# Optimization experiments

Hardware: AMD Instinct MI355X
Metric: run time of the kernel (lower is better)

The kernel has to match this reference:

```python
import jax, jax.numpy as jnp
import numpy as np

B, S, H = 128, 512, 1024
SEP = 2


def setup_inputs() -> dict:
    key = jax.random.key(0)
    k1, k2, k3, k4 = jax.random.split(key, 4)
    hidden_states = jax.random.normal(k1, (B, S, H), dtype=jnp.float32)
    # per-sample segment boundaries: <s> title </s></s> lead </s> pad...
    title_end = jax.random.randint(k2, (B,), 5, 200)          # pos of first </s>
    lead_end = jax.random.randint(k3, (B,), 250, S - 2)        # pos of third </s>
    tokens = jax.random.randint(k4, (B, S), 5, 64000)          # avoid SEP=2 collisions
    rows = jnp.arange(B)
    input_ids = tokens.at[:, 0].set(0)                          # <s>
    input_ids = input_ids.at[rows, title_end].set(SEP)
    input_ids = input_ids.at[rows, title_end + 1].set(SEP)
    input_ids = input_ids.at[rows, lead_end].set(SEP)
    attention_mask = (jnp.arange(S)[None, :] <= lead_end[:, None]).astype(jnp.int32)
    return {
        "hidden_states": hidden_states,
        "input_ids": input_ids.astype(jnp.int64),
        "attention_mask": attention_mask,
        "sep_token_id": SEP,
    }


def reference(hidden_states, input_ids, attention_mask, sep_token_id):
    # hidden_states: (B,S,H); input_ids, attention_mask: (B,S)
    b, s, h = hidden_states.shape
    sep = input_ids == sep_token_id                      # (B,S) bool
    cnt = jnp.cumsum(sep.astype(jnp.int32), axis=1)      # inclusive sep count
    num_seps = cnt[:, -1]                                # (B,)

    def pos_of(k):
        # index of k-th separator (argmax of first True); 0 if absent
        return jnp.argmax(sep & (cnt == k), axis=1)

    p1, p2, p3 = pos_of(1), pos_of(2), pos_of(3)
    mask_len = attention_mask.sum(axis=1)
    lead_end = jnp.where(num_seps >= 3, p3, mask_len)    # (B,)
    lead_start = p2 + 1

    idx = jnp.arange(s)[None, :]                         # (1,S)
    valid = (num_seps >= 2)[:, None]
    title_mask = (idx >= 1) & (idx < p1[:, None]) & valid
    lead_mask = (idx >= lead_start[:, None]) & (idx < lead_end[:, None]) & valid

    cls = hidden_states[:, 0, :]                         # fallback: <s> token

    def masked_mean(m):
        mf = m.astype(hidden_states.dtype)               # (B,S)
        ssum = jnp.einsum('bs,bsh->bh', mf, hidden_states)
        c = mf.sum(axis=1, keepdims=True)                # (B,1)
        return jnp.where(c > 0, ssum / jnp.maximum(c, 1.0), cls)

    return masked_mean(title_mask), masked_mean(lead_mask)
```

## Files before the change

kernel.cpp:

```cpp
#include <hip/hip_runtime.h>

#define BB 128
#define SS 512
#define HH 1024
#define CHUNKS 16
#define SCHUNK (SS / CHUNKS)

__device__ __forceinline__ int4 compute_meta(const int* __restrict__ ids,
                                             const int* __restrict__ attn,
                                             int b, int sep) {
    __shared__ unsigned long long words[SS / 64];
    __shared__ int sh_p[4];
    __shared__ int sh_mask;
    const int t = threadIdx.x;
    const int* row = ids + b * SS;
    const int tok0 = row[t];
    const int tok1 = row[t + 256];
    const unsigned long long b0 = __ballot(tok0 == sep);
    const unsigned long long b1 = __ballot(tok1 == sep);
    if ((t & 63) == 0) {
        words[t >> 6] = b0;
        words[4 + (t >> 6)] = b1;
    }
    if (t == 0) sh_mask = 0;
    __syncthreads();
    if (t == 0) {
        int cnt = 0, p1 = 0, p2 = 0, p3 = 0;
        for (int i = 0; i < SS / 64; ++i) {
            unsigned long long word = words[i];
            while (word && cnt < 3) {
                const int pos = i * 64 + __builtin_ctzll(word);
                ++cnt;
                if (cnt == 1) p1 = pos;
                else if (cnt == 2) p2 = pos;
                else p3 = pos;
                word &= word - 1;
            }
        }
        sh_p[0] = p1; sh_p[1] = p2; sh_p[2] = p3; sh_p[3] = cnt;
    }
    __syncthreads();
    const int cnt = sh_p[3];
    if (cnt < 3) {
        const int* arow = attn + b * SS;
        atomicAdd(&sh_mask, arow[t] + arow[t + 256]);
        __syncthreads();
    }
    int4 m;
    if (cnt >= 2) {
        m.x = 1;
        m.y = max(sh_p[0], 1);
        m.z = sh_p[1] + 1;
        const int e = (cnt >= 3) ? sh_p[2] : sh_mask;
        m.w = max(e, m.z);
    } else {
        m.x = 0; m.y = 0; m.z = 0; m.w = 0;
    }
    return m;
}

__device__ __forceinline__ void acc4(float4& a, const float4 v) {
    a.x += v.x; a.y += v.y; a.z += v.z; a.w += v.w;
}

__global__ void seg_sum_partial(const float* __restrict__ hs,
                                const int* __restrict__ ids,
                                const int* __restrict__ attn,
                                const int* __restrict__ sep_tok,
                                float* __restrict__ partials) {
    const int c = blockIdx.x;
    const int b = blockIdx.y;
    const int4 m = compute_meta(ids, attn, b, sep_tok[0]);

    const int cbeg = c * SCHUNK, cend = cbeg + SCHUNK;
    const int t0 = max(m.x, cbeg), t1 = min(m.y, cend);
    const int l0 = max(m.z, cbeg), l1 = min(m.w, cend);
    const bool ht = t1 > t0, hl = l1 > l0;
    if (!ht && !hl) return;

    const int h4 = threadIdx.x;
    const float4* base = (const float4*)(hs + (size_t)b * SS * HH);
    float4* pbase = (float4*)(partials + (size_t)(b * CHUNKS + c) * 2 * HH);

    if (ht) {
        float4 a = {0.f, 0.f, 0.f, 0.f};
        #pragma unroll 4
        for (int s = t0; s < t1; ++s) acc4(a, base[(size_t)s * (HH / 4) + h4]);
        pbase[h4] = a;
    }
    if (hl) {
        float4 a = {0.f, 0.f, 0.f, 0.f};
        #pragma unroll 4
        for (int s = l0; s < l1; ++s) acc4(a, base[(size_t)s * (HH / 4) + h4]);
        pbase[HH / 4 + h4] = a;
    }
}

__global__ void seg_final_partial(const float* __restrict__ hs,
                                  const int* __restrict__ ids,
                                  const int* __restrict__ attn,
                                  const int* __restrict__ sep_tok,
                                  const float* __restrict__ partials,
                                  float* __restrict__ out) {
    const int span = blockIdx.x;
    const int b = blockIdx.y;
    const int4 m = compute_meta(ids, attn, b, sep_tok[0]);
    const int h4 = threadIdx.x;

    const int s0 = span == 0 ? m.x : m.z;
    const int s1 = span == 0 ? m.y : m.w;

    float4 a = {0.f, 0.f, 0.f, 0.f};
    #pragma unroll
    for (int c = 0; c < CHUNKS; ++c) {
        const int cbeg = c * SCHUNK, cend = cbeg + SCHUNK;
        const int x0 = max(s0, cbeg), x1 = min(s1, cend);
        if (x1 > x0) {
            const float4* p = (const float4*)(partials +
                (size_t)(b * CHUNKS + c) * 2 * HH + (size_t)span * HH);
            acc4(a, p[h4]);
        }
    }

    const int cntr = max(s1 - s0, 0);
    float4 o;
    if (cntr > 0) {
        const float c = (float)cntr;
        o.x = a.x / c; o.y = a.y / c; o.z = a.z / c; o.w = a.w / c;
    } else {
        o = ((const float4*)(hs + (size_t)b * SS * HH))[h4];
    }
    ((float4*)out)[(size_t)(span * BB + b) * (HH / 4) + h4] = o;
}

__global__ void seg_sum_atomic(const float* __restrict__ hs,
                               const int* __restrict__ ids,
                               const int* __restrict__ attn,
                               const int* __restrict__ sep_tok,
                               float* __restrict__ sums) {
    const int c = blockIdx.x;
    const int b = blockIdx.y;
    const int4 m = compute_meta(ids, attn, b, sep_tok[0]);

    const int cbeg = c * SCHUNK, cend = cbeg + SCHUNK;
    const int t0 = max(m.x, cbeg), t1 = min(m.y, cend);
    const int l0 = max(m.z, cbeg), l1 = min(m.w, cend);
    if (t0 >= t1 && l0 >= l1) return;

    const int h4 = threadIdx.x;
    const float4* base = (const float4*)(hs + (size_t)b * SS * HH);
    float* sbase = sums + (size_t)b * 2 * HH;

    if (t1 > t0) {
        float4 a = {0.f, 0.f, 0.f, 0.f};
        #pragma unroll 4
        for (int s = t0; s < t1; ++s) acc4(a, base[(size_t)s * (HH / 4) + h4]);
        atomicAdd(sbase + h4 * 4 + 0, a.x); atomicAdd(sbase + h4 * 4 + 1, a.y);
        atomicAdd(sbase + h4 * 4 + 2, a.z); atomicAdd(sbase + h4 * 4 + 3, a.w);
    }
    if (l1 > l0) {
        float4 a = {0.f, 0.f, 0.f, 0.f};
        #pragma unroll 4
        for (int s = l0; s < l1; ++s) acc4(a, base[(size_t)s * (HH / 4) + h4]);
        float* sl = sbase + HH;
        atomicAdd(sl + h4 * 4 + 0, a.x); atomicAdd(sl + h4 * 4 + 1, a.y);
        atomicAdd(sl + h4 * 4 + 2, a.z); atomicAdd(sl + h4 * 4 + 3, a.w);
    }
}

__global__ void seg_final_atomic(const float* __restrict__ hs,
                                 const int* __restrict__ ids,
                                 const int* __restrict__ attn,
                                 const int* __restrict__ sep_tok,
                                 const float* __restrict__ sums,
                                 float* __restrict__ out) {
    const int span = blockIdx.x;
    const int b = blockIdx.y;
    const int4 m = compute_meta(ids, attn, b, sep_tok[0]);
    const int h4 = threadIdx.x;

    const int s0 = span == 0 ? m.x : m.z;
    const int s1 = span == 0 ? m.y : m.w;
    const int cntr = max(s1 - s0, 0);

    float4 o;
    if (cntr > 0) {
        const float4 a = ((const float4*)(sums + (size_t)b * 2 * HH + (size_t)span * HH))[h4];
        const float c = (float)cntr;
        o.x = a.x / c; o.y = a.y / c; o.z = a.z / c; o.w = a.w / c;
    } else {
        o = ((const float4*)(hs + (size_t)b * SS * HH))[h4];
    }
    ((float4*)out)[(size_t)(span * BB + b) * (HH / 4) + h4] = o;
}

extern "C" void kernel_launch(void* const* d_in, const int* in_sizes, int n_in,
                              void* d_out, int out_size, void* d_ws, size_t ws_size,
                              hipStream_t stream) {
    const float* hs  = (const float*)d_in[0];
    const int*   ids = (const int*)d_in[1];
    const int*   am  = (const int*)d_in[2];
    const int*   sep = (const int*)d_in[3];
    float* out = (float*)d_out;

    const size_t partial_bytes = (size_t)BB * CHUNKS * 2 * HH * sizeof(float);

    if (ws_size >= partial_bytes) {
        float* partials = (float*)d_ws;
        seg_sum_partial<<<dim3(CHUNKS, BB), 256, 0, stream>>>(hs, ids, am, sep, partials);
        seg_final_partial<<<dim3(2, BB), 256, 0, stream>>>(hs, ids, am, sep, partials, out);
    } else {
        float* sums = (float*)d_ws;
        hipMemsetAsync(sums, 0, (size_t)BB * 2 * HH * sizeof(float), stream);
        seg_sum_atomic<<<dim3(CHUNKS, BB), 256, 0, stream>>>(hs, ids, am, sep, sums);
        seg_final_atomic<<<dim3(2, BB), 256, 0, stream>>>(hs, ids, am, sep, sums, out);
    }
}
```

Before: 47.18 us.

## Load-balance segment rows across blocks with strided interleaving and nontemporal loads

```diff
diff --git a/kernel.cpp b/kernel.cpp
--- a/kernel.cpp
+++ b/kernel.cpp
@@ -3,8 +3,9 @@
 #define BB 128
 #define SS 512
 #define HH 1024
-#define CHUNKS 16
-#define SCHUNK (SS / CHUNKS)
+#define NB 16
+
+typedef float f32x4 __attribute__((ext_vector_type(4)));
 
 __device__ __forceinline__ int4 compute_meta(const int* __restrict__ ids,
                                              const int* __restrict__ attn,
@@ -59,139 +60,91 @@
     return m;
 }
 
-__device__ __forceinline__ void acc4(float4& a, const float4 v) {
-    a.x += v.x; a.y += v.y; a.z += v.z; a.w += v.w;
+__device__ __forceinline__ int lead_first_u(int t_len, int nb) {
+    int d = nb - (t_len % NB);
+    if (d < 0) d += NB;
+    return t_len + d;
 }
 
-__global__ void seg_sum_partial(const float* __restrict__ hs,
-                                const int* __restrict__ ids,
-                                const int* __restrict__ attn,
-                                const int* __restrict__ sep_tok,
-                                float* __restrict__ partials) {
-    const int c = blockIdx.x;
-    const int b = blockIdx.y;
+__global__ void seg_sum_balanced(const float* __restrict__ hs,
+                                 const int* __restrict__ ids,
+                                 const int* __restrict__ attn,
+                                 const int* __restrict__ sep_tok,
+                                 float* __restrict__ partials) {
+    const int nb = blockIdx.x;
+    const int b  = blockIdx.y;
     const int4 m = compute_meta(ids, attn, b, sep_tok[0]);
-
-    const int cbeg = c * SCHUNK, cend = cbeg + SCHUNK;
-    const int t0 = max(m.x, cbeg), t1 = min(m.y, cend);
-    const int l0 = max(m.z, cbeg), l1 = min(m.w, cend);
-    const bool ht = t1 > t0, hl = l1 > l0;
-    if (!ht && !hl) return;
+    const int t_len = m.y - m.x;
+    const int l_len = m.w - m.z;
+    const int T = t_len + l_len;
 
     const int h4 = threadIdx.x;
-    const float4* base = (const float4*)(hs + (size_t)b * SS * HH);
-    float4* pbase = (float4*)(partials + (size_t)(b * CHUNKS + c) * 2 * HH);
+    const f32x4* base = (const f32x4*)(hs + (size_t)b * SS * HH);
+    f32x4* p = (f32x4*)(partials + (size_t)(b * NB + nb) * 2 * HH);
 
-    if (ht) {
-        float4 a = {0.f, 0.f, 0.f, 0.f};
-        #pragma unroll 4
-        for (int s = t0; s < t1; ++s) acc4(a, base[(size_t)s * (HH / 4) + h4]);
-        pbase[h4] = a;
+    if (nb < t_len) {
+        f32x4 a = {0.f, 0.f, 0.f, 0.f};
+        #pragma unroll 2
+        for (int u = nb; u < t_len; u += NB) {
+            const int s = m.x + u;
+            a += __builtin_nontemporal_load(&base[(size_t)s * (HH / 4) + h4]);
+        }
+        p[h4] = a;
     }
-    if (hl) {
-        float4 a = {0.f, 0.f, 0.f, 0.f};
-        #pragma unroll 4
-        for (int s = l0; s < l1; ++s) acc4(a, base[(size_t)s * (HH / 4) + h4]);
-        pbase[HH / 4 + h4] = a;
+    const int u0 = lead_first_u(t_len, nb);
+    if (u0 < T) {
+        f32x4 a = {0.f, 0.f, 0.f, 0.f};
+        #pragma unroll 2
+        for (int u = u0; u < T; u += NB) {
+            const int s = m.z + (u - t_len);
+            a += __builtin_nontemporal_load(&base[(size_t)s * (HH / 4) + h4]);
+        }
+        p[HH / 4 + h4] = a;
     }
 }
 
-__global__ void seg_final_partial(const float* __restrict__ hs,
-                                  const int* __restrict__ ids,
-                                  const int* __restrict__ attn,
-                                  const int* __restrict__ sep_tok,
-                                  const float* __restrict__ partials,
-                                  float* __restrict__ out) {
+__global__ void seg_final_balanced(const float* __restrict__ hs,
+                                   const int* __restrict__ ids,
+                                   const int* __restrict__ attn,
+                                   const int* __restrict__ sep_tok,
+                                   const float* __restrict__ partials,
+                                   float* __restrict__ out) {
     const int span = blockIdx.x;
     const int b = blockIdx.y;
     const int4 m = compute_meta(ids, attn, b, sep_tok[0]);
     const int h4 = threadIdx.x;
+    const int t_len = m.y - m.x;
+    const int l_len = m.w - m.z;
+    const int T = t_len + l_len;
 
-    const int s0 = span == 0 ? m.x : m.z;
-    const int s1 = span == 0 ? m.y : m.w;
-
-    float4 a = {0.f, 0.f, 0.f, 0.f};
-    #pragma unroll
-    for (int c = 0; c < CHUNKS; ++c) {
-        const int cbeg = c * SCHUNK, cend = cbeg + SCHUNK;
-        const int x0 = max(s0, cbeg), x1 = min(s1, cend);
-        if (x1 > x0) {
-            const float4* p = (const float4*)(partials +
-                (size_t)(b * CHUNKS + c) * 2 * HH + (size_t)span * HH);
-            acc4(a, p[h4]);
+    f32x4 a = {0.f, 0.f, 0.f, 0.f};
+    int cntr;
+    if (span == 0) {
+        cntr = t_len;
+        const int lim = min(t_len, NB);
+        for (int nb = 0; nb < lim; ++nb) {
+            const f32x4* p = (const f32x4*)(partials + (size_t)(b * NB + nb) * 2 * HH);
+            a += p[h4];
+        }
+    } else {
+        cntr = l_len;
+        #pragma unroll
+        for (int nb = 0; nb < NB; ++nb) {
+            if (lead_first_u(t_len, nb) < T) {
+                const f32x4* p = (const f32x4*)(partials + (size_t)(b * NB + nb) * 2 * HH);
+                a += p[HH / 4 + h4];
+            }
         }
     }
 
-    const int cntr = max(s1 - s0, 0);
-    float4 o;
+    f32x4 o;
     if (cntr > 0) {
         const float c = (float)cntr;
-        o.x = a.x / c; o.y = a.y / c; o.z = a.z / c; o.w = a.w / c;
+        o = a / c;
     } else {
-        o = ((const float4*)(hs + (size_t)b * SS * HH))[h4];
+        o = ((const f32x4*)(hs + (size_t)b * SS * HH))[h4];
     }
-    ((float4*)out)[(size_t)(span * BB + b) * (HH / 4) + h4] = o;
-}
-
-__global__ void seg_sum_atomic(const float* __restrict__ hs,
-                               const int* __restrict__ ids,
-                               const int* __restrict__ attn,
-                               const int* __restrict__ sep_tok,
-                               float* __restrict__ sums) {
-    const int c = blockIdx.x;
-    const int b = blockIdx.y;
-    const int4 m = compute_meta(ids, attn, b, sep_tok[0]);
-
-    const int cbeg = c * SCHUNK, cend = cbeg + SCHUNK;
-    const int t0 = max(m.x, cbeg), t1 = min(m.y, cend);
-    const int l0 = max(m.z, cbeg), l1 = min(m.w, cend);
-    if (t0 >= t1 && l0 >= l1) return;
-
-    const int h4 = threadIdx.x;
-    const float4* base = (const float4*)(hs + (size_t)b * SS * HH);
-    float* sbase = sums + (size_t)b * 2 * HH;
-
-    if (t1 > t0) {
-        float4 a = {0.f, 0.f, 0.f, 0.f};
-        #pragma unroll 4
-        for (int s = t0; s < t1; ++s) acc4(a, base[(size_t)s * (HH / 4) + h4]);
-        atomicAdd(sbase + h4 * 4 + 0, a.x); atomicAdd(sbase + h4 * 4 + 1, a.y);
-        atomicAdd(sbase + h4 * 4 + 2, a.z); atomicAdd(sbase + h4 * 4 + 3, a.w);
-    }
-    if (l1 > l0) {
-        float4 a = {0.f, 0.f, 0.f, 0.f};
-        #pragma unroll 4
-        for (int s = l0; s < l1; ++s) acc4(a, base[(size_t)s * (HH / 4) + h4]);
-        float* sl = sbase + HH;
-        atomicAdd(sl + h4 * 4 + 0, a.x); atomicAdd(sl + h4 * 4 + 1, a.y);
-        atomicAdd(sl + h4 * 4 + 2, a.z); atomicAdd(sl + h4 * 4 + 3, a.w);
-    }
-}
-
-__global__ void seg_final_atomic(const float* __restrict__ hs,
-                                 const int* __restrict__ ids,
-                                 const int* __restrict__ attn,
-                                 const int* __restrict__ sep_tok,
-                                 const float* __restrict__ sums,
-                                 float* __restrict__ out) {
-    const int span = blockIdx.x;
-    const int b = blockIdx.y;
-    const int4 m = compute_meta(ids, attn, b, sep_tok[0]);
-    const int h4 = threadIdx.x;
-
-    const int s0 = span == 0 ? m.x : m.z;
-    const int s1 = span == 0 ? m.y : m.w;
-    const int cntr = max(s1 - s0, 0);
-
-    float4 o;
-    if (cntr > 0) {
-        const float4 a = ((const float4*)(sums + (size_t)b * 2 * HH + (size_t)span * HH))[h4];
-        const float c = (float)cntr;
-        o.x = a.x / c; o.y = a.y / c; o.z = a.z / c; o.w = a.w / c;
-    } else {
-        o = ((const float4*)(hs + (size_t)b * SS * HH))[h4];
-    }
-    ((float4*)out)[(size_t)(span * BB + b) * (HH / 4) + h4] = o;
+    ((f32x4*)out)[(size_t)(span * BB + b) * (HH / 4) + h4] = o;
 }
 
 extern "C" void kernel_launch(void* const* d_in, const int* in_sizes, int n_in,
@@ -202,17 +155,8 @@
     const int*   am  = (const int*)d_in[2];
     const int*   sep = (const int*)d_in[3];
     float* out = (float*)d_out;
+    float* partials = (float*)d_ws;
 
-    const size_t partial_bytes = (size_t)BB * CHUNKS * 2 * HH * sizeof(float);
-
-    if (ws_size >= partial_bytes) {
-        float* partials = (float*)d_ws;
-        seg_sum_partial<<<dim3(CHUNKS, BB), 256, 0, stream>>>(hs, ids, am, sep, partials);
-        seg_final_partial<<<dim3(2, BB), 256, 0, stream>>>(hs, ids, am, sep, partials, out);
-    } else {
-        float* sums = (float*)d_ws;
-        hipMemsetAsync(sums, 0, (size_t)BB * 2 * HH * sizeof(float), stream);
-        seg_sum_atomic<<<dim3(CHUNKS, BB), 256, 0, stream>>>(hs, ids, am, sep, sums);
-        seg_final_atomic<<<dim3(2, BB), 256, 0, stream>>>(hs, ids, am, sep, sums, out);
-    }
+    seg_sum_balanced<<<dim3(NB, BB), 256, 0, stream>>>(hs, ids, am, sep, partials);
+    seg_final_balanced<<<dim3(2, BB), 256, 0, stream>>>(hs, ids, am, sep, partials, out);
 }
```

Measured after the change: 53.64 us. 1.14x slower.
